# Kernel tuning notes

Measured on AMD Instinct MI355X. Metric: run time of the kernel, lower is better.

The kernel has to match this reference:

```python
import jax, jax.numpy as jnp
import numpy as np

D_MODEL, D_INNER, D_STATE, D_CONV, DT_RANK = 512, 1024, 16, 4, 32
B, L = 2, 2048
EPS = 1e-5


def setup_inputs() -> dict:
    key = jax.random.key(0)
    ks = jax.random.split(key, 10)
    s = 0.02
    return {
        "x": jax.random.normal(ks[0], (B, L, D_MODEL), jnp.float32),
        "attention_mask": jnp.ones((B, L), jnp.int32),
        "norm_weight": jnp.ones((D_MODEL,), jnp.float32),
        "in_proj_w": jax.random.normal(ks[1], (2 * D_INNER, D_MODEL), jnp.float32) * s,
        "conv_w": jax.random.normal(ks[2], (D_INNER, 1, D_CONV), jnp.float32) * 0.3,
        "conv_b": jnp.zeros((D_INNER,), jnp.float32),
        "x_proj_w": jax.random.normal(ks[3], (DT_RANK + 2 * D_STATE, D_INNER), jnp.float32) * s,
        "dt_proj_w": jax.random.normal(ks[4], (D_INNER, DT_RANK), jnp.float32) * 0.1,
        "dt_proj_b": jnp.full((D_INNER,), -4.6, jnp.float32),  # softplus ~ 0.01
        "A_log": jnp.log(jnp.tile(jnp.arange(1, D_STATE + 1, dtype=jnp.float32), (D_INNER, 1))),
        "D": jnp.ones((D_INNER,), jnp.float32),
        "out_proj_w": jax.random.normal(ks[5], (D_MODEL, D_INNER), jnp.float32) * s,
    }


def _mamba_block(h, in_proj_w, conv_w, conv_b, x_proj_w, dt_proj_w, dt_proj_b, A_log, D, out_proj_w):
    # in_proj -> split into x, z  (B, L, D_INNER) each
    xz = jnp.einsum("bld,ed->ble", h, in_proj_w)
    u, z = jnp.split(xz, 2, axis=-1)
    # causal depthwise conv over time, then SiLU
    u_ncl = jnp.transpose(u, (0, 2, 1))  # (B, D_INNER, L)
    conv = jax.lax.conv_general_dilated(
        u_ncl, conv_w, window_strides=(1,), padding=[(D_CONV - 1, 0)],
        feature_group_count=D_INNER, dimension_numbers=("NCH", "OIH", "NCH"))
    u = jax.nn.silu(jnp.transpose(conv + conv_b[None, :, None], (0, 2, 1)))  # (B, L, D_INNER)
    # x_proj -> dt (low rank), Bm, Cm
    xdbc = jnp.einsum("bld,ed->ble", u, x_proj_w)
    dt_r, Bm, Cm = jnp.split(xdbc, [DT_RANK, DT_RANK + D_STATE], axis=-1)
    dt = jax.nn.softplus(jnp.einsum("blr,dr->bld", dt_r, dt_proj_w) + dt_proj_b)  # (B,L,D_INNER)
    A = -jnp.exp(A_log)  # (D_INNER, D_STATE)

    def step(hstate, inputs):
        dt_t, B_t, C_t, u_t = inputs  # (B,Din), (B,Dst), (B,Dst), (B,Din)
        dA = jnp.exp(dt_t[..., None] * A)                      # (B, Din, Dst)
        dBu = dt_t[..., None] * B_t[:, None, :] * u_t[..., None]
        hstate = dA * hstate + dBu
        y_t = jnp.einsum("bds,bs->bd", hstate, C_t)
        return hstate, y_t

    xs = (jnp.swapaxes(dt, 0, 1), jnp.swapaxes(Bm, 0, 1), jnp.swapaxes(Cm, 0, 1), jnp.swapaxes(u, 0, 1))
    h0 = jnp.zeros((u.shape[0], D_INNER, D_STATE), u.dtype)
    _, ys = jax.lax.scan(step, h0, xs)
    y = jnp.swapaxes(ys, 0, 1) + D * u          # skip term
    y = y * jax.nn.silu(z)                      # gating
    return jnp.einsum("ble,de->bld", y, out_proj_w)


def reference(x, attention_mask, norm_weight, in_proj_w, conv_w, conv_b,
              x_proj_w, dt_proj_w, dt_proj_b, A_log, D, out_proj_w):
    # pre-norm RMSNorm
    var = jnp.mean(jnp.square(x), axis=-1, keepdims=True)
    h = x * jax.lax.rsqrt(var + EPS) * norm_weight
    mask = attention_mask[..., None].astype(h.dtype)
    h = h * mask
    h = _mamba_block(h, in_proj_w, conv_w, conv_b, x_proj_w, dt_proj_w, dt_proj_b, A_log, D, out_proj_w)
    h = h * mask
    return x + h
```

## Files before the change

### kernel.cpp

```cpp
#include <hip/hip_runtime.h>
#include <hip/hip_bf16.h>
#include <math.h>

#define D_MODEL 512
#define D_INNER 1024
#define D_STATE 16
#define DT_RANK 32
#define B_SZ 2
#define SEQ 2048
#define ROWS (B_SZ*SEQ)
#define EPSV 1e-5f
#define NCHUNK 64
#define CLEN (SEQ/NCHUNK)
#define NPAIR (B_SZ*D_INNER)
#define LOG2E 1.44269504088896f
#define N_ALL 1152

typedef short bf16x8 __attribute__((ext_vector_type(8)));
typedef float f32x4  __attribute__((ext_vector_type(4)));
typedef __hip_bfloat16 bf16_t;

static __device__ __forceinline__ float bf2f(bf16_t v) { return __bfloat162float(v); }
static __device__ __forceinline__ float bfraw2f(short v) {
    return __uint_as_float(((unsigned)(unsigned short)v) << 16);
}

static __device__ __forceinline__ void xcd_swizzle(int& bx, int& by) {
    int gx = gridDim.x;
    int nwg = gx * gridDim.y;
    int flat = by * gx + bx;
    int q = nwg >> 3;
    int s = (flat & 7) * q + (flat >> 3);
    bx = s % gx; by = s / gx;
}

__global__ __launch_bounds__(256) void prep_kernel(
        const float* __restrict__ in_proj_w, const float* __restrict__ out_proj_w,
        const float* __restrict__ dt_proj_w, const float* __restrict__ x_proj_w,
        const float* __restrict__ x, const int* __restrict__ mask,
        const float* __restrict__ norm_w,
        bf16_t* __restrict__ w_in, bf16_t* __restrict__ w_out,
        bf16_t* __restrict__ W_all, bf16_t* __restrict__ h) {
    int bid = blockIdx.x;
    int tid = threadIdx.x;
    if (bid < 1536) {
        const float* src = (bid < 1024) ? in_proj_w : out_proj_w;
        bf16_t* dst = (bid < 1024) ? w_in : w_out;
        int i = ((bid < 1024) ? bid : (bid - 1024)) * 256 + tid;
        float4 v = reinterpret_cast<const float4*>(src)[i];
        bf16_t o[4] = {__float2bfloat16(v.x), __float2bfloat16(v.y),
                       __float2bfloat16(v.z), __float2bfloat16(v.w)};
        reinterpret_cast<ushort4*>(dst)[i] = *reinterpret_cast<ushort4*>(o);
    } else if (bid < 1792) {
        __shared__ float a[64][33];
        __shared__ float b[32][68];
        int blk = bid - 1536;
        int n0 = (blk >> 4) * 64;
        int k0 = (blk & 15) * 64;
        #pragma unroll
        for (int hh = 0; hh < 2; ++hh) {
            int q = tid + hh * 256;
            int r = q >> 3, c = (q & 7) * 4;
            float4 v = *reinterpret_cast<const float4*>(dt_proj_w + (size_t)(n0 + r) * DT_RANK + c);
            a[r][c] = v.x; a[r][c + 1] = v.y; a[r][c + 2] = v.z; a[r][c + 3] = v.w;
            int r2 = q >> 4, c2 = (q & 15) * 4;
            float4 w = *reinterpret_cast<const float4*>(x_proj_w + (size_t)r2 * D_INNER + k0 + c2);
            b[r2][c2] = w.x; b[r2][c2 + 1] = w.y; b[r2][c2 + 2] = w.z; b[r2][c2 + 3] = w.w;
        }
        __syncthreads();
        int ty = tid >> 4, tx = tid & 15;
        float acc[4][4] = {};
        #pragma unroll
        for (int r = 0; r < 32; ++r) {
            float av[4], bv[4];
            #pragma unroll
            for (int i = 0; i < 4; ++i) av[i] = a[ty * 4 + i][r];
            #pragma unroll
            for (int j = 0; j < 4; ++j) bv[j] = b[r][tx * 4 + j];
            #pragma unroll
            for (int i = 0; i < 4; ++i)
                #pragma unroll
                for (int j = 0; j < 4; ++j)
                    acc[i][j] = fmaf(av[i], bv[j], acc[i][j]);
        }
        #pragma unroll
        for (int i = 0; i < 4; ++i) {
            bf16_t o[4];
            #pragma unroll
            for (int j = 0; j < 4; ++j) o[j] = __float2bfloat16(acc[i][j]);
            *reinterpret_cast<ushort4*>(W_all + (size_t)(n0 + ty * 4 + i) * D_INNER + k0 + tx * 4) =
                *reinterpret_cast<ushort4*>(o);
        }
    } else if (bid < 1920) {
        int row = bid - 1792;
        int cq = tid * 4;
        bf16_t o[4] = {};
        if (row < 32) {
            float4 v = *reinterpret_cast<const float4*>(x_proj_w + (size_t)(32 + row) * D_INNER + cq);
            o[0] = __float2bfloat16(v.x); o[1] = __float2bfloat16(v.y);
            o[2] = __float2bfloat16(v.z); o[3] = __float2bfloat16(v.w);
        }
        *reinterpret_cast<ushort4*>(W_all + (size_t)(1024 + row) * D_INNER + cq) =
            *reinterpret_cast<ushort4*>(o);
    } else {
        __shared__ float red[4];
        int row = bid - 1920;
        const float2 v = reinterpret_cast<const float2*>(x + (size_t)row * D_MODEL)[tid];
        float ss = v.x * v.x + v.y * v.y;
        #pragma unroll
        for (int m = 1; m < 64; m <<= 1) ss += __shfl_xor(ss, m);
        if ((tid & 63) == 0) red[tid >> 6] = ss;
        __syncthreads();
        float tot = red[0] + red[1] + red[2] + red[3];
        float scale = rsqrtf(tot * (1.0f / D_MODEL) + EPSV) * (float)mask[row];
        __hip_bfloat162 o;
        o.x = __float2bfloat16(v.x * scale * norm_w[2 * tid]);
        o.y = __float2bfloat16(v.y * scale * norm_w[2 * tid + 1]);
        reinterpret_cast<__hip_bfloat162*>(h + (size_t)row * D_MODEL)[tid] = o;
    }
}

template<int MODE, int TN>
__global__ __launch_bounds__(256, 2) void gemm_mfma(
        const bf16_t* __restrict__ A, const bf16_t* __restrict__ Bw,
        void* __restrict__ Cv, int M, int N, int K,
        const float* __restrict__ xres, const int* __restrict__ mask2,
        void* __restrict__ z2, const float* __restrict__ bias) {
    constexpr int MI  = (TN == 128) ? 4 : 2;
    constexpr int BCH = TN / 32;
    __shared__ alignas(16) bf16_t As[2][128 * 64];
    __shared__ alignas(16) bf16_t Bs[2][TN * 64];
    const int tid = threadIdx.x;
    const int wid = tid >> 6, lane = tid & 63;
    int bx = blockIdx.x, by = blockIdx.y;
    xcd_swizzle(bx, by);
    const int m0 = by * 128, n0 = bx * TN;
    const int wr = (TN == 128) ? ((wid >> 1) * 64) : (wid * 32);
    const int wc = (TN == 128) ? ((wid & 1) * 64) : 0;

    f32x4 acc[MI][4];
    #pragma unroll
    for (int i = 0; i < MI; ++i)
        #pragma unroll
        for (int j = 0; j < 4; ++j)
            #pragma unroll
            for (int r = 0; r < 4; ++r) acc[i][j][r] = 0.f;

    const int rrow = lane & 15, kg = lane >> 4;
    const int lrow = lane >> 3;
    const int cbs = (lane & 7) ^ lrow;

    int offA[2][MI], offB[2][4];
    #pragma unroll
    for (int kk = 0; kk < 2; ++kk) {
        #pragma unroll
        for (int i = 0; i < MI; ++i) {
            int ra = wr + i * 16 + rrow;
            offA[kk][i] = ra * 64 + (((kk * 4 + kg) ^ (ra & 7)) * 8);
        }
        #pragma unroll
        for (int j = 0; j < 4; ++j) {
            int rb = wc + j * 16 + rrow;
            offB[kk][j] = rb * 64 + (((kk * 4 + kg) ^ (rb & 7)) * 8);
        }
    }
    const bf16_t* gAp[4];
    const bf16_t* gBp[BCH];
    #pragma unroll
    for (int j = 0; j < 4; ++j) {
        int r = (wid * 4 + j) * 8 + lrow;
        gAp[j] = A + (size_t)(m0 + r) * K + cbs * 8;
    }
    #pragma unroll
    for (int j = 0; j < BCH; ++j) {
        int r = (wid * BCH + j) * 8 + lrow;
        gBp[j] = Bw + (size_t)(n0 + r) * K + cbs * 8;
    }

    auto stage = [&](bf16_t* AS, bf16_t* BS) {
        #pragma unroll
        for (int j = 0; j < 4; ++j) {
            int c = wid * 4 + j;
            __builtin_amdgcn_global_load_lds(
                (const __attribute__((address_space(1))) void*)gAp[j],
                (__attribute__((address_space(3))) void*)(AS + c * 512), 16, 0, 0);
            gAp[j] += 64;
        }
        #pragma unroll
        for (int j = 0; j < BCH; ++j) {
            int c = wid * BCH + j;
            __builtin_amdgcn_global_load_lds(
                (const __attribute__((address_space(1))) void*)gBp[j],
                (__attribute__((address_space(3))) void*)(BS + c * 512), 16, 0, 0);
            gBp[j] += 64;
        }
    };
    auto compute = [&](const bf16_t* AS, const bf16_t* BS) {
        #pragma unroll
        for (int kk = 0; kk < 2; ++kk) {
            bf16x8 af[MI], bfr[4];
            #pragma unroll
            for (int i = 0; i < MI; ++i)
                af[i] = *reinterpret_cast<const bf16x8*>(AS + offA[kk][i]);
            #pragma unroll
            for (int j = 0; j < 4; ++j)
                bfr[j] = *reinterpret_cast<const bf16x8*>(BS + offB[kk][j]);
            #pragma unroll
            for (int i = 0; i < MI; ++i)
                #pragma unroll
                for (int j = 0; j < 4; ++j)
                    acc[i][j] = __builtin_amdgcn_mfma_f32_16x16x32_bf16(bfr[j], af[i], acc[i][j], 0, 0, 0);
        }
    };

    stage(As[0], Bs[0]);
    __syncthreads();
    for (int k0 = 0; k0 < K; k0 += 128) {
        stage(As[1], Bs[1]);
        compute(As[0], Bs[0]);
        __syncthreads();
        if (k0 + 128 < K) stage(As[0], Bs[0]);
        compute(As[1], Bs[1]);
        __syncthreads();
    }

    #pragma unroll
    for (int i = 0; i < MI; ++i) {
        int m = m0 + wr + i * 16 + (lane & 15);
        #pragma unroll
        for (int j = 0; j < 4; ++j) {
            int nb = n0 + wc + j * 16 + (lane >> 4) * 4;
            f32x4 v = acc[i][j];
            if (MODE == 2) {
                float mf = (float)mask2[m];
                float4 xr = *reinterpret_cast<const float4*>(xres + (size_t)m * N + nb);
                float4 o;
                o.x = xr.x + mf * v[0]; o.y = xr.y + mf * v[1];
                o.z = xr.z + mf * v[2]; o.w = xr.w + mf * v[3];
                *reinterpret_cast<float4*>((float*)Cv + (size_t)m * N + nb) = o;
            } else if (MODE == 3) {
                bf16_t o[4];
                if (nb < D_INNER) {
                    #pragma unroll
                    for (int r = 0; r < 4; ++r) o[r] = __float2bfloat16(v[r]);
                    *reinterpret_cast<ushort4*>((bf16_t*)Cv + (size_t)m * D_INNER + nb) =
                        *reinterpret_cast<ushort4*>(o);
                } else {
                    #pragma unroll
                    for (int r = 0; r < 4; ++r) {
                        float zv = v[r];
                        o[r] = __float2bfloat16(zv / (1.f + __expf(-zv)));
                    }
                    *reinterpret_cast<ushort4*>((bf16_t*)z2 + (size_t)m * D_INNER + (nb - D_INNER)) =
                        *reinterpret_cast<ushort4*>(o);
                }
            } else {
                if (nb < D_INNER) {
                    float4 bs = *reinterpret_cast<const float4*>(bias + nb);
                    float s0 = v[0] + bs.x, s1 = v[1] + bs.y, s2 = v[2] + bs.z, s3 = v[3] + bs.w;
                    s0 = (s0 > 20.f) ? s0 : __logf(1.f + __expf(s0));
                    s1 = (s1 > 20.f) ? s1 : __logf(1.f + __expf(s1));
                    s2 = (s2 > 20.f) ? s2 : __logf(1.f + __expf(s2));
                    s3 = (s3 > 20.f) ? s3 : __logf(1.f + __expf(s3));
                    bf16_t o[4] = {__float2bfloat16(s0), __float2bfloat16(s1),
                                   __float2bfloat16(s2), __float2bfloat16(s3)};
                    *reinterpret_cast<ushort4*>((bf16_t*)Cv + (size_t)m * D_INNER + nb) =
                        *reinterpret_cast<ushort4*>(o);
                } else if (nb < D_INNER + 32) {
                    float4 o; o.x = v[0]; o.y = v[1]; o.z = v[2]; o.w = v[3];
                    *reinterpret_cast<float4*>((float*)z2 + (size_t)m * 32 + (nb - D_INNER)) = o;
                }
            }
        }
    }
}

__global__ __launch_bounds__(256) void conv_silu_kernel(const bf16_t* __restrict__ upre,
        const float* __restrict__ conv_w, const float* __restrict__ conv_b,
        bf16_t* __restrict__ u) {
    int idx = blockIdx.x * 256 + threadIdx.x;
    int dq = idx & 127;
    int row = idx >> 7;
    int t = row & (SEQ - 1);
    int d0 = dq * 8;
    const bf16_t* base = upre + (size_t)(row - t) * D_INNER + d0;
    float s_[8];
    {
        float4 b0 = *reinterpret_cast<const float4*>(conv_b + d0);
        float4 b1 = *reinterpret_cast<const float4*>(conv_b + d0 + 4);
        s_[0] = b0.x; s_[1] = b0.y; s_[2] = b0.z; s_[3] = b0.w;
        s_[4] = b1.x; s_[5] = b1.y; s_[6] = b1.z; s_[7] = b1.w;
    }
    #pragma unroll
    for (int j = 0; j < 4; ++j) {
        int tt = t - 3 + j;
        if (tt >= 0) {
            bf16x8 vv = *reinterpret_cast<const bf16x8*>(base + (size_t)tt * D_INNER);
            #pragma unroll
            for (int i = 0; i < 8; ++i)
                s_[i] = fmaf(conv_w[(d0 + i) * 4 + j], bfraw2f(vv[i]), s_[i]);
        }
    }
    bf16_t o[8];
    #pragma unroll
    for (int i = 0; i < 8; ++i) {
        float v = s_[i];
        o[i] = __float2bfloat16(v / (1.f + __expf(-v)));
    }
    *reinterpret_cast<bf16x8*>(u + (size_t)row * D_INNER + d0) =
        *reinterpret_cast<bf16x8*>(o);
}

__global__ __launch_bounds__(256) void scan_phase1(
        const bf16_t* __restrict__ dtb, const bf16_t* __restrict__ ub,
        const float* __restrict__ bcbuf, const float* __restrict__ A_log,
        float* __restrict__ P, float* __restrict__ F) {
    int tid = threadIdx.x;
    int bid = blockIdx.x;
    int dblk = bid & 7, c = (bid >> 3) & (NCHUNK - 1), b = bid >> 9;
    int d = dblk * 128 + (tid >> 1);
    int sh = (tid & 1) * 8;
    __shared__ float sBC[CLEN][32];
    size_t rb = (size_t)b * SEQ + (size_t)c * CLEN;
    {
        int row = tid >> 3, q = tid & 7;
        *reinterpret_cast<float4*>(&sBC[row][q * 4]) =
            *reinterpret_cast<const float4*>(bcbuf + (rb + row) * 32 + q * 4);
    }
    float A2[8];
    #pragma unroll
    for (int s4 = 0; s4 < 2; ++s4) {
        float4 a = *reinterpret_cast<const float4*>(A_log + d * D_STATE + sh + s4 * 4);
        A2[s4 * 4 + 0] = -expf(a.x) * LOG2E;
        A2[s4 * 4 + 1] = -expf(a.y) * LOG2E;
        A2[s4 * 4 + 2] = -expf(a.z) * LOG2E;
        A2[s4 * 4 + 3] = -expf(a.w) * LOG2E;
    }
    float p[8], f[8];
    #pragma unroll
    for (int s = 0; s < 8; ++s) { p[s] = 1.f; f[s] = 0.f; }
    const bf16_t* dtp = dtb + rb * D_INNER + d;
    const bf16_t* up  = ub  + rb * D_INNER + d;
    float dtc[4], uc[4];
    #pragma unroll
    for (int j = 0; j < 4; ++j) {
        dtc[j] = bf2f(dtp[(size_t)j * D_INNER]);
        uc[j]  = bf2f(up[(size_t)j * D_INNER]);
    }
    __syncthreads();
    for (int tb = 0; tb < CLEN; tb += 4) {
        float dtn[4], un[4];
        if (tb + 4 < CLEN) {
            #pragma unroll
            for (int j = 0; j < 4; ++j) {
                dtn[j] = bf2f(dtp[(size_t)(tb + 4 + j) * D_INNER]);
                un[j]  = bf2f(up[(size_t)(tb + 4 + j) * D_INNER]);
            }
        } else {
            #pragma unroll
            for (int j = 0; j < 4; ++j) { dtn[j] = 0.f; un[j] = 0.f; }
        }
        #pragma unroll
        for (int j = 0; j < 4; ++j) {
            float dtv = dtc[j];
            float dtu = dtv * uc[j];
            #pragma unroll
            for (int s = 0; s < 8; ++s) {
                float e = exp2f(dtv * A2[s]);
                p[s] *= e;
                f[s] = fmaf(e, f[s], sBC[tb + j][sh + s] * dtu);
            }
        }
        #pragma unroll
        for (int j = 0; j < 4; ++j) { dtc[j] = dtn[j]; uc[j] = un[j]; }
    }
    size_t o = ((size_t)(b * D_INNER + d) * NCHUNK + c) * D_STATE + sh;
    #pragma unroll
    for (int s4 = 0; s4 < 2; ++s4) {
        float4 vp = {p[s4*4+0], p[s4*4+1], p[s4*4+2], p[s4*4+3]};
        float4 vf = {f[s4*4+0], f[s4*4+1], f[s4*4+2], f[s4*4+3]};
        *reinterpret_cast<float4*>(P + o + s4 * 4) = vp;
        *reinterpret_cast<float4*>(F + o + s4 * 4) = vf;
    }
}

__global__ __launch_bounds__(256) void scan_phase2(
        float* __restrict__ P, const float* __restrict__ F) {
    int idx = blockIdx.x * 256 + threadIdx.x;
    int pair = idx >> 4, s = idx & 15;
    size_t base = (size_t)pair * NCHUNK * D_STATE + s;
    float pp[8], ff[8];
    #pragma unroll
    for (int j = 0; j < 8; ++j) {
        pp[j] = P[base + (size_t)j * D_STATE];
        ff[j] = F[base + (size_t)j * D_STATE];
    }
    float h = 0.f;
    #pragma unroll
    for (int cb = 0; cb < 8; ++cb) {
        #pragma unroll
        for (int j = 0; j < 8; ++j) {
            int c = cb * 8 + j;
            float p = pp[j], f = ff[j];
            if (cb < 7) {
                pp[j] = P[base + (size_t)(c + 8) * D_STATE];
                ff[j] = F[base + (size_t)(c + 8) * D_STATE];
            }
            P[base + (size_t)c * D_STATE] = h;
            h = fmaf(p, h, f);
        }
    }
}

__global__ __launch_bounds__(256) void scan_phase3(
        const bf16_t* __restrict__ dtb, const bf16_t* __restrict__ ub,
        const float* __restrict__ bcbuf, const bf16_t* __restrict__ gbuf,
        const float* __restrict__ A_log, const float* __restrict__ Dw,
        const float* __restrict__ Hinit, bf16_t* __restrict__ ybuf) {
    int tid = threadIdx.x;
    int bid = blockIdx.x;
    int dblk = bid & 7, c = (bid >> 3) & (NCHUNK - 1), b = bid >> 9;
    int d = dblk * 128 + (tid >> 1);
    int sh = (tid & 1) * 8;
    __shared__ float sBC[CLEN][32];
    size_t rb = (size_t)b * SEQ + (size_t)c * CLEN;
    {
        int row = tid >> 3, q = tid & 7;
        *reinterpret_cast<float4*>(&sBC[row][q * 4]) =
            *reinterpret_cast<const float4*>(bcbuf + (rb + row) * 32 + q * 4);
    }
    float A2[8];
    #pragma unroll
    for (int s4 = 0; s4 < 2; ++s4) {
        float4 a = *reinterpret_cast<const float4*>(A_log + d * D_STATE + sh + s4 * 4);
        A2[s4 * 4 + 0] = -expf(a.x) * LOG2E;
        A2[s4 * 4 + 1] = -expf(a.y) * LOG2E;
        A2[s4 * 4 + 2] = -expf(a.z) * LOG2E;
        A2[s4 * 4 + 3] = -expf(a.w) * LOG2E;
    }
    float Dd = Dw[d];
    float st[8];
    size_t o = ((size_t)(b * D_INNER + d) * NCHUNK + c) * D_STATE + sh;
    #pragma unroll
    for (int s4 = 0; s4 < 2; ++s4) {
        float4 hv = *reinterpret_cast<const float4*>(Hinit + o + s4 * 4);
        st[s4*4+0] = hv.x; st[s4*4+1] = hv.y; st[s4*4+2] = hv.z; st[s4*4+3] = hv.w;
    }
    const bf16_t* dtp = dtb + rb * D_INNER + d;
    const bf16_t* up  = ub  + rb * D_INNER + d;
    const bf16_t* gp  = gbuf + rb * D_INNER + d;
    bf16_t* yp = ybuf + rb * D_INNER + d;
    float dtc[4], uc[4], gc[4];
    #pragma unroll
    for (int j = 0; j < 4; ++j) {
        dtc[j] = bf2f(dtp[(size_t)j * D_INNER]);
        uc[j]  = bf2f(up[(size_t)j * D_INNER]);
        gc[j]  = bf2f(gp[(size_t)j * D_INNER]);
    }
    __syncthreads();
    for (int tb = 0; tb < CLEN; tb += 4) {
        float dtn[4], un[4], gn[4];
        if (tb + 4 < CLEN) {
            #pragma unroll
            for (int j = 0; j < 4; ++j) {
                dtn[j] = bf2f(dtp[(size_t)(tb + 4 + j) * D_INNER]);
                un[j]  = bf2f(up[(size_t)(tb + 4 + j) * D_INNER]);
                gn[j]  = bf2f(gp[(size_t)(tb + 4 + j) * D_INNER]);
            }
        } else {
            #pragma unroll
            for (int j = 0; j < 4; ++j) { dtn[j] = 0.f; un[j] = 0.f; gn[j] = 0.f; }
        }
        #pragma unroll
        for (int j = 0; j < 4; ++j) {
            float dtv = dtc[j];
            float dtu = dtv * uc[j];
            float y = 0.f;
            #pragma unroll
            for (int s = 0; s < 8; ++s) {
                float e = exp2f(dtv * A2[s]);
                st[s] = fmaf(e, st[s], sBC[tb + j][sh + s] * dtu);
                y = fmaf(st[s], sBC[tb + j][16 + sh + s], y);
            }
            y += __shfl_xor(y, 1);
            if ((tid & 1) == 0) {
                yp[(size_t)(tb + j) * D_INNER] =
                    __float2bfloat16((y + Dd * uc[j]) * gc[j]);
            }
        }
        #pragma unroll
        for (int j = 0; j < 4; ++j) { dtc[j] = dtn[j]; uc[j] = un[j]; gc[j] = gn[j]; }
    }
}

extern "C" void kernel_launch(void* const* d_in, const int* in_sizes, int n_in,
                              void* d_out, int out_size, void* d_ws, size_t ws_size,
                              hipStream_t stream) {
    const float* x          = (const float*)d_in[0];
    const int*   mask       = (const int*)d_in[1];
    const float* norm_w     = (const float*)d_in[2];
    const float* in_proj_w  = (const float*)d_in[3];
    const float* conv_w     = (const float*)d_in[4];
    const float* conv_b     = (const float*)d_in[5];
    const float* x_proj_w   = (const float*)d_in[6];
    const float* dt_proj_w  = (const float*)d_in[7];
    const float* dt_proj_b  = (const float*)d_in[8];
    const float* A_log      = (const float*)d_in[9];
    const float* Dw         = (const float*)d_in[10];
    const float* out_proj_w = (const float*)d_in[11];
    float* out = (float*)d_out;
    float* ws  = (float*)d_ws;

    bf16_t* u_pre = (bf16_t*)ws;
    bf16_t* gbuf  = (bf16_t*)(ws + 2097152);
    bf16_t* u_bf  = (bf16_t*)(ws + 6291456);
    bf16_t* dt_bf = (bf16_t*)(ws + 8388608);
    bf16_t* h_bf  = (bf16_t*)(ws + 10485760);
    bf16_t* y_bf  = (bf16_t*)(ws + 10485760);
    float*  bcbuf = ws + 12582912;
    float*  Pbuf  = ws + 12845056;
    bf16_t* w_in  = (bf16_t*)(ws + 12845056);
    float*  Fbuf  = ws + 14942208;
    bf16_t* W_all = (bf16_t*)(ws + 14942208);
    bf16_t* w_out = (bf16_t*)(ws + 17039360);

    prep_kernel<<<6016, 256, 0, stream>>>(in_proj_w, out_proj_w, dt_proj_w, x_proj_w,
                                          x, mask, norm_w, w_in, w_out, W_all, h_bf);
    gemm_mfma<3, 128><<<dim3(16, 32), 256, 0, stream>>>(
        h_bf, w_in, u_pre, ROWS, 2 * D_INNER, D_MODEL, nullptr, nullptr, gbuf, nullptr);
    conv_silu_kernel<<<(ROWS * D_INNER / 8) / 256, 256, 0, stream>>>(u_pre, conv_w, conv_b, u_bf);
    gemm_mfma<4, 128><<<dim3(N_ALL / 128, 32), 256, 0, stream>>>(
        u_bf, W_all, dt_bf, ROWS, N_ALL, D_INNER, nullptr, nullptr, bcbuf, dt_proj_b);
    scan_phase1<<<B_SZ * NCHUNK * 8, 256, 0, stream>>>(dt_bf, u_bf, bcbuf, A_log, Pbuf, Fbuf);
    scan_phase2<<<NPAIR * D_STATE / 256, 256, 0, stream>>>(Pbuf, Fbuf);
    scan_phase3<<<B_SZ * NCHUNK * 8, 256, 0, stream>>>(dt_bf, u_bf, bcbuf, gbuf, A_log, Dw,
                                                       Pbuf, y_bf);
    gemm_mfma<2, 64><<<dim3(8, 32), 256, 0, stream>>>(
        y_bf, w_out, out, ROWS, D_MODEL, D_INNER, x, mask, nullptr, nullptr);
}
```

Before: 164.1 us.

## Store dt and gate transposed so scan kernels read contiguous time vectors

The in_proj and x_proj GEMMs now write the gate (silu z) and dt outputs in channel-major (transposed) layout. They do this by swapping the MFMA operand order for those tiles, so each lane holds four consecutive rows. The scan phase kernels then load 8 timesteps of dt and gate with one 16-byte vector load instead of strided scalar loads, and the time loop is unrolled by 8 instead of 4. This trades more register pressure, and transposed stores of 8-byte chunks strided by ROWS, for far fewer strided global loads in the scan.

```diff
diff --git a/kernel.cpp b/kernel.cpp
--- a/kernel.cpp
+++ b/kernel.cpp
@@ -138,6 +138,9 @@
     const int wr = (TN == 128) ? ((wid >> 1) * 64) : (wid * 32);
     const int wc = (TN == 128) ? ((wid & 1) * 64) : 0;
 
+    const bool ns = (MODE == 3) ? (n0 >= D_INNER)
+                  : (MODE == 4) ? (n0 < D_INNER) : false;
+
     f32x4 acc[MI][4];
     #pragma unroll
     for (int i = 0; i < MI; ++i)
@@ -195,7 +198,7 @@
             gBp[j] += 64;
         }
     };
-    auto compute = [&](const bf16_t* AS, const bf16_t* BS) {
+    auto computeS = [&](const bf16_t* AS, const bf16_t* BS) {
         #pragma unroll
         for (int kk = 0; kk < 2; ++kk) {
             bf16x8 af[MI], bfr[4];
@@ -212,63 +215,100 @@
                     acc[i][j] = __builtin_amdgcn_mfma_f32_16x16x32_bf16(bfr[j], af[i], acc[i][j], 0, 0, 0);
         }
     };
-
-    stage(As[0], Bs[0]);
-    __syncthreads();
-    for (int k0 = 0; k0 < K; k0 += 128) {
-        stage(As[1], Bs[1]);
-        compute(As[0], Bs[0]);
+    auto computeNS = [&](const bf16_t* AS, const bf16_t* BS) {
+        #pragma unroll
+        for (int kk = 0; kk < 2; ++kk) {
+            bf16x8 af[MI], bfr[4];
+            #pragma unroll
+            for (int i = 0; i < MI; ++i)
+                af[i] = *reinterpret_cast<const bf16x8*>(AS + offA[kk][i]);
+            #pragma unroll
+            for (int j = 0; j < 4; ++j)
+                bfr[j] = *reinterpret_cast<const bf16x8*>(BS + offB[kk][j]);
+            #pragma unroll
+            for (int i = 0; i < MI; ++i)
+                #pragma unroll
+                for (int j = 0; j < 4; ++j)
+                    acc[i][j] = __builtin_amdgcn_mfma_f32_16x16x32_bf16(af[i], bfr[j], acc[i][j], 0, 0, 0);
+        }
+    };
+
+    if (ns) {
+        stage(As[0], Bs[0]);
         __syncthreads();
-        if (k0 + 128 < K) stage(As[0], Bs[0]);
-        compute(As[1], Bs[1]);
+        for (int k0 = 0; k0 < K; k0 += 128) {
+            stage(As[1], Bs[1]);
+            computeNS(As[0], Bs[0]);
+            __syncthreads();
+            if (k0 + 128 < K) stage(As[0], Bs[0]);
+            computeNS(As[1], Bs[1]);
+            __syncthreads();
+        }
+        #pragma unroll
+        for (int i = 0; i < MI; ++i) {
+            int mb = m0 + wr + i * 16 + (lane >> 4) * 4;
+            #pragma unroll
+            for (int j = 0; j < 4; ++j) {
+                int n = n0 + wc + j * 16 + (lane & 15);
+                f32x4 v = acc[i][j];
+                bf16_t o[4];
+                if (MODE == 3) {
+                    #pragma unroll
+                    for (int r = 0; r < 4; ++r) {
+                        float zv = v[r];
+                        o[r] = __float2bfloat16(zv / (1.f + __expf(-zv)));
+                    }
+                    *reinterpret_cast<ushort4*>((bf16_t*)z2 + (size_t)(n - D_INNER) * ROWS + mb) =
+                        *reinterpret_cast<ushort4*>(o);
+                } else {
+                    float bs = bias[n];
+                    #pragma unroll
+                    for (int r = 0; r < 4; ++r) {
+                        float s = v[r] + bs;
+                        s = (s > 20.f) ? s : __logf(1.f + __expf(s));
+                        o[r] = __float2bfloat16(s);
+                    }
+                    *reinterpret_cast<ushort4*>((bf16_t*)Cv + (size_t)n * ROWS + mb) =
+                        *reinterpret_cast<ushort4*>(o);
+                }
+            }
+        }
+    } else {
+        stage(As[0], Bs[0]);
         __syncthreads();
-    }
-
-    #pragma unroll
-    for (int i = 0; i < MI; ++i) {
-        int m = m0 + wr + i * 16 + (lane & 15);
-        #pragma unroll
-        for (int j = 0; j < 4; ++j) {
-            int nb = n0 + wc + j * 16 + (lane >> 4) * 4;
-            f32x4 v = acc[i][j];
-            if (MODE == 2) {
-                float mf = (float)mask2[m];
-                float4 xr = *reinterpret_cast<const float4*>(xres + (size_t)m * N + nb);
-                float4 o;
-                o.x = xr.x + mf * v[0]; o.y = xr.y + mf * v[1];
-                o.z = xr.z + mf * v[2]; o.w = xr.w + mf * v[3];
-                *reinterpret_cast<float4*>((float*)Cv + (size_t)m * N + nb) = o;
-            } else if (MODE == 3) {
-                bf16_t o[4];
-                if (nb < D_INNER) {
+        for (int k0 = 0; k0 < K; k0 += 128) {
+            stage(As[1], Bs[1]);
+            computeS(As[0], Bs[0]);
+            __syncthreads();
+            if (k0 + 128 < K) stage(As[0], Bs[0]);
+            computeS(As[1], Bs[1]);
+            __syncthreads();
+        }
+        #pragma unroll
+        for (int i = 0; i < MI; ++i) {
+            int m = m0 + wr + i * 16 + (lane & 15);
+            #pragma unroll
+            for (int j = 0; j < 4; ++j) {
+                int nb = n0 + wc + j * 16 + (lane >> 4) * 4;
+                f32x4 v = acc[i][j];
+                if (MODE == 2) {
+                    float mf = (float)mask2[m];
+                    float4 xr = *reinterpret_cast<const float4*>(xres + (size_t)m * N + nb);
+                    float4 o;
+                    o.x = xr.x + mf * v[0]; o.y = xr.y + mf * v[1];
+                    o.z = xr.z + mf * v[2]; o.w = xr.w + mf * v[3];
+                    *reinterpret_cast<float4*>((float*)Cv + (size_t)m * N + nb) = o;
+                } else if (MODE == 3) {
+                    bf16_t o[4];
                     #pragma unroll
                     for (int r = 0; r < 4; ++r) o[r] = __float2bfloat16(v[r]);
                     *reinterpret_cast<ushort4*>((bf16_t*)Cv + (size_t)m * D_INNER + nb) =
                         *reinterpret_cast<ushort4*>(o);
                 } else {
-                    #pragma unroll
-                    for (int r = 0; r < 4; ++r) {
-                        float zv = v[r];
-                        o[r] = __float2bfloat16(zv / (1.f + __expf(-zv)));
+                    if (nb < D_INNER + 32) {
+                        float4 o; o.x = v[0]; o.y = v[1]; o.z = v[2]; o.w = v[3];
+                        *reinterpret_cast<float4*>((float*)z2 + (size_t)m * 32 + (nb - D_INNER)) = o;
                     }
-                    *reinterpret_cast<ushort4*>((bf16_t*)z2 + (size_t)m * D_INNER + (nb - D_INNER)) =
-                        *reinterpret_cast<ushort4*>(o);
-                }
-            } else {
-                if (nb < D_INNER) {
-                    float4 bs = *reinterpret_cast<const float4*>(bias + nb);
-                    float s0 = v[0] + bs.x, s1 = v[1] + bs.y, s2 = v[2] + bs.z, s3 = v[3] + bs.w;
-                    s0 = (s0 > 20.f) ? s0 : __logf(1.f + __expf(s0));
-                    s1 = (s1 > 20.f) ? s1 : __logf(1.f + __expf(s1));
-                    s2 = (s2 > 20.f) ? s2 : __logf(1.f + __expf(s2));
-                    s3 = (s3 > 20.f) ? s3 : __logf(1.f + __expf(s3));
-                    bf16_t o[4] = {__float2bfloat16(s0), __float2bfloat16(s1),
-                                   __float2bfloat16(s2), __float2bfloat16(s3)};
-                    *reinterpret_cast<ushort4*>((bf16_t*)Cv + (size_t)m * D_INNER + nb) =
-                        *reinterpret_cast<ushort4*>(o);
-                } else if (nb < D_INNER + 32) {
-                    float4 o; o.x = v[0]; o.y = v[1]; o.z = v[2]; o.w = v[3];
-                    *reinterpret_cast<float4*>((float*)z2 + (size_t)m * 32 + (nb - D_INNER)) = o;
                 }
             }
         }
@@ -312,7 +352,7 @@
 }
 
 __global__ __launch_bounds__(256) void scan_phase1(
-        const bf16_t* __restrict__ dtb, const bf16_t* __restrict__ ub,
+        const bf16_t* __restrict__ dtT, const bf16_t* __restrict__ ub,
         const float* __restrict__ bcbuf, const float* __restrict__ A_log,
         float* __restrict__ P, float* __restrict__ F) {
     int tid = threadIdx.x;
@@ -339,31 +379,28 @@
     float p[8], f[8];
     #pragma unroll
     for (int s = 0; s < 8; ++s) { p[s] = 1.f; f[s] = 0.f; }
-    const bf16_t* dtp = dtb + rb * D_INNER + d;
-    const bf16_t* up  = ub  + rb * D_INNER + d;
-    float dtc[4], uc[4];
-    #pragma unroll
-    for (int j = 0; j < 4; ++j) {
-        dtc[j] = bf2f(dtp[(size_t)j * D_INNER]);
-        uc[j]  = bf2f(up[(size_t)j * D_INNER]);
-    }
+    const bf16_t* dtp = dtT + (size_t)d * ROWS + rb;
+    const bf16_t* up  = ub + rb * D_INNER + d;
+    bf16x8 dtA = *reinterpret_cast<const bf16x8*>(dtp);
+    float uA[8];
+    #pragma unroll
+    for (int j = 0; j < 8; ++j) uA[j] = bf2f(up[(size_t)j * D_INNER]);
     __syncthreads();
-    for (int tb = 0; tb < CLEN; tb += 4) {
-        float dtn[4], un[4];
-        if (tb + 4 < CLEN) {
-            #pragma unroll
-            for (int j = 0; j < 4; ++j) {
-                dtn[j] = bf2f(dtp[(size_t)(tb + 4 + j) * D_INNER]);
-                un[j]  = bf2f(up[(size_t)(tb + 4 + j) * D_INNER]);
-            }
+    for (int tb = 0; tb < CLEN; tb += 8) {
+        bf16x8 dtB = dtA;
+        float uB[8];
+        if (tb + 8 < CLEN) {
+            dtB = *reinterpret_cast<const bf16x8*>(dtp + tb + 8);
+            #pragma unroll
+            for (int j = 0; j < 8; ++j) uB[j] = bf2f(up[(size_t)(tb + 8 + j) * D_INNER]);
         } else {
             #pragma unroll
-            for (int j = 0; j < 4; ++j) { dtn[j] = 0.f; un[j] = 0.f; }
-        }
-        #pragma unroll
-        for (int j = 0; j < 4; ++j) {
-            float dtv = dtc[j];
-            float dtu = dtv * uc[j];
+            for (int j = 0; j < 8; ++j) uB[j] = 0.f;
+        }
+        #pragma unroll
+        for (int j = 0; j < 8; ++j) {
+            float dtv = bfraw2f(dtA[j]);
+            float dtu = dtv * uA[j];
             #pragma unroll
             for (int s = 0; s < 8; ++s) {
                 float e = exp2f(dtv * A2[s]);
@@ -371,8 +408,9 @@
                 f[s] = fmaf(e, f[s], sBC[tb + j][sh + s] * dtu);
             }
         }
-        #pragma unroll
-        for (int j = 0; j < 4; ++j) { dtc[j] = dtn[j]; uc[j] = un[j]; }
+        dtA = dtB;
+        #pragma unroll
+        for (int j = 0; j < 8; ++j) uA[j] = uB[j];
     }
     size_t o = ((size_t)(b * D_INNER + d) * NCHUNK + c) * D_STATE + sh;
     #pragma unroll
@@ -413,8 +451,8 @@
 }
 
 __global__ __launch_bounds__(256) void scan_phase3(
-        const bf16_t* __restrict__ dtb, const bf16_t* __restrict__ ub,
-        const float* __restrict__ bcbuf, const bf16_t* __restrict__ gbuf,
+        const bf16_t* __restrict__ dtT, const bf16_t* __restrict__ ub,
+        const float* __restrict__ bcbuf, const bf16_t* __restrict__ gT,
         const float* __restrict__ A_log, const float* __restrict__ Dw,
         const float* __restrict__ Hinit, bf16_t* __restrict__ ybuf) {
     int tid = threadIdx.x;
@@ -446,35 +484,32 @@
         float4 hv = *reinterpret_cast<const float4*>(Hinit + o + s4 * 4);
         st[s4*4+0] = hv.x; st[s4*4+1] = hv.y; st[s4*4+2] = hv.z; st[s4*4+3] = hv.w;
     }
-    const bf16_t* dtp = dtb + rb * D_INNER + d;
-    const bf16_t* up  = ub  + rb * D_INNER + d;
-    const bf16_t* gp  = gbuf + rb * D_INNER + d;
+    const bf16_t* dtp = dtT + (size_t)d * ROWS + rb;
+    const bf16_t* gp  = gT  + (size_t)d * ROWS + rb;
+    const bf16_t* up  = ub + rb * D_INNER + d;
     bf16_t* yp = ybuf + rb * D_INNER + d;
-    float dtc[4], uc[4], gc[4];
-    #pragma unroll
-    for (int j = 0; j < 4; ++j) {
-        dtc[j] = bf2f(dtp[(size_t)j * D_INNER]);
-        uc[j]  = bf2f(up[(size_t)j * D_INNER]);
-        gc[j]  = bf2f(gp[(size_t)j * D_INNER]);
-    }
+    bf16x8 dtA = *reinterpret_cast<const bf16x8*>(dtp);
+    bf16x8 gA  = *reinterpret_cast<const bf16x8*>(gp);
+    float uA[8];
+    #pragma unroll
+    for (int j = 0; j < 8; ++j) uA[j] = bf2f(up[(size_t)j * D_INNER]);
     __syncthreads();
-    for (int tb = 0; tb < CLEN; tb += 4) {
-        float dtn[4], un[4], gn[4];
-        if (tb + 4 < CLEN) {
-            #pragma unroll
-            for (int j = 0; j < 4; ++j) {
-                dtn[j] = bf2f(dtp[(size_t)(tb + 4 + j) * D_INNER]);
-                un[j]  = bf2f(up[(size_t)(tb + 4 + j) * D_INNER]);
-                gn[j]  = bf2f(gp[(size_t)(tb + 4 + j) * D_INNER]);
-            }
+    for (int tb = 0; tb < CLEN; tb += 8) {
+        bf16x8 dtB = dtA, gB = gA;
+        float uB[8];
+        if (tb + 8 < CLEN) {
+            dtB = *reinterpret_cast<const bf16x8*>(dtp + tb + 8);
+            gB  = *reinterpret_cast<const bf16x8*>(gp + tb + 8);
+            #pragma unroll
+            for (int j = 0; j < 8; ++j) uB[j] = bf2f(up[(size_t)(tb + 8 + j) * D_INNER]);
         } else {
             #pragma unroll
-            for (int j = 0; j < 4; ++j) { dtn[j] = 0.f; un[j] = 0.f; gn[j] = 0.f; }
-        }
-        #pragma unroll
-        for (int j = 0; j < 4; ++j) {
-            float dtv = dtc[j];
-            float dtu = dtv * uc[j];
+            for (int j = 0; j < 8; ++j) uB[j] = 0.f;
+        }
+        #pragma unroll
+        for (int j = 0; j < 8; ++j) {
+            float dtv = bfraw2f(dtA[j]);
+            float dtu = dtv * uA[j];
             float y = 0.f;
             #pragma unroll
             for (int s = 0; s < 8; ++s) {
@@ -485,11 +520,12 @@
             y += __shfl_xor(y, 1);
             if ((tid & 1) == 0) {
                 yp[(size_t)(tb + j) * D_INNER] =
-                    __float2bfloat16((y + Dd * uc[j]) * gc[j]);
+                    __float2bfloat16((y + Dd * uA[j]) * bfraw2f(gA[j]));
             }
         }
-        #pragma unroll
-        for (int j = 0; j < 4; ++j) { dtc[j] = dtn[j]; uc[j] = un[j]; gc[j] = gn[j]; }
+        dtA = dtB; gA = gB;
+        #pragma unroll
+        for (int j = 0; j < 8; ++j) uA[j] = uB[j];
     }
 }
 
@@ -512,9 +548,9 @@
     float* ws  = (float*)d_ws;
 
     bf16_t* u_pre = (bf16_t*)ws;
-    bf16_t* gbuf  = (bf16_t*)(ws + 2097152);
+    bf16_t* gT    = (bf16_t*)(ws + 2097152);
     bf16_t* u_bf  = (bf16_t*)(ws + 6291456);
-    bf16_t* dt_bf = (bf16_t*)(ws + 8388608);
+    bf16_t* dtT   = (bf16_t*)(ws + 8388608);
     bf16_t* h_bf  = (bf16_t*)(ws + 10485760);
     bf16_t* y_bf  = (bf16_t*)(ws + 10485760);
     float*  bcbuf = ws + 12582912;
@@ -527,13 +563,13 @@
     prep_kernel<<<6016, 256, 0, stream>>>(in_proj_w, out_proj_w, dt_proj_w, x_proj_w,
                                           x, mask, norm_w, w_in, w_out, W_all, h_bf);
     gemm_mfma<3, 128><<<dim3(16, 32), 256, 0, stream>>>(
-        h_bf, w_in, u_pre, ROWS, 2 * D_INNER, D_MODEL, nullptr, nullptr, gbuf, nullptr);
+        h_bf, w_in, u_pre, ROWS, 2 * D_INNER, D_MODEL, nullptr, nullptr, gT, nullptr);
     conv_silu_kernel<<<(ROWS * D_INNER / 8) / 256, 256, 0, stream>>>(u_pre, conv_w, conv_b, u_bf);
     gemm_mfma<4, 128><<<dim3(N_ALL / 128, 32), 256, 0, stream>>>(
-        u_bf, W_all, dt_bf, ROWS, N_ALL, D_INNER, nullptr, nullptr, bcbuf, dt_proj_b);
-    scan_phase1<<<B_SZ * NCHUNK * 8, 256, 0, stream>>>(dt_bf, u_bf, bcbuf, A_log, Pbuf, Fbuf);
+        u_bf, W_all, dtT, ROWS, N_ALL, D_INNER, nullptr, nullptr, bcbuf, dt_proj_b);
+    scan_phase1<<<B_SZ * NCHUNK * 8, 256, 0, stream>>>(dtT, u_bf, bcbuf, A_log, Pbuf, Fbuf);
     scan_phase2<<<NPAIR * D_STATE / 256, 256, 0, stream>>>(Pbuf, Fbuf);
-    scan_phase3<<<B_SZ * NCHUNK * 8, 256, 0, stream>>>(dt_bf, u_bf, bcbuf, gbuf, A_log, Dw,
+    scan_phase3<<<B_SZ * NCHUNK * 8, 256, 0, stream>>>(dtT, u_bf, bcbuf, gT, A_log, Dw,
                                                        Pbuf, y_bf);
     gemm_mfma<2, 64><<<dim3(8, 32), 256, 0, stream>>>(
         y_bf, w_out, out, ROWS, D_MODEL, D_INNER, x, mask, nullptr, nullptr);
```

New measurement: 159.1 us. 1.03x faster.
